# Optimization experiments

Hardware: AMD Instinct MI355X
Metric: run time of the kernel (lower is better)

The kernel has to match this reference:

```python
import jax, jax.numpy as jnp
import numpy as np
from jax import lax

B, CIN, COUT, K, SDIM = 4, 64, 128, 3, 512
D = H = W = 48


def setup_inputs() -> dict:
    key = jax.random.key(0)
    ks = jax.random.split(key, 8)
    inv = lambda n: 1.0 / np.sqrt(n)
    return {
        "x": jax.random.normal(ks[0], (B, CIN, D, H, W), jnp.float32),
        "style": jax.random.normal(ks[1], (B, SDIM), jnp.float32),
        "weight": jax.random.normal(ks[2], (COUT, CIN, K, K, K), jnp.float32),
        "bias": jnp.zeros((COUT,), jnp.float32),
        "w_scale": jax.random.uniform(ks[3], (CIN, SDIM), jnp.float32, -inv(SDIM), inv(SDIM)),
        "b_scale": jnp.zeros((CIN,), jnp.float32),
        "w_shift": jax.random.uniform(ks[4], (CIN, SDIM), jnp.float32, -inv(SDIM), inv(SDIM)),
        "b_shift": jnp.zeros((CIN,), jnp.float32),
        "w_kmod": jax.random.uniform(ks[5], (CIN * K ** 3, SDIM), jnp.float32, -inv(SDIM), inv(SDIM)),
        "b_kmod": jnp.zeros((CIN * K ** 3,), jnp.float32),
    }


def reference(x, style, weight, bias, w_scale, b_scale, w_shift, b_shift, w_kmod, b_kmod):
    # style-based per-channel input modulation: x * (1+scale) + shift
    scale = style @ w_scale.T + b_scale          # [B, CIN]
    shift = style @ w_shift.T + b_shift          # [B, CIN]
    xm = x * (1.0 + scale)[:, :, None, None, None] + shift[:, :, None, None, None]
    # per-sample kernel modulation: weight * (1 + kmod)
    kmod = (style @ w_kmod.T + b_kmod).reshape(B, CIN, K, K, K)
    w = weight[None] * (1.0 + kmod[:, None])     # [B, COUT, CIN, K, K, K]

    def conv_one(xi, wi):
        # xi: [CIN, D, H, W], wi: [COUT, CIN, K, K, K]
        return lax.conv_general_dilated(
            xi[None], wi, window_strides=(1, 1, 1), padding="SAME",
            dimension_numbers=("NCDHW", "OIDHW", "NCDHW"))[0]

    out = jax.vmap(conv_one)(xm, w)              # [B, COUT, D, H, W]
    return out + bias[None, :, None, None, None]
```

## Files before the change

### kernel.cpp

```cpp
#include <hip/hip_runtime.h>
#include <hip/hip_bf16.h>

#define NB   4
#define CIN  64
#define COUT 128
#define SDIM 512
#define DIM  48
#define SP   (DIM*DIM*DIM)
#define TAPS 27
#define KTOT (CIN*TAPS)

#define WS_S1P 0
#define WS_SH  (WS_S1P + NB*CIN)
#define WS_KM  (WS_SH + NB*CIN)
#define XPB_OFF   32768ull
#define XPB_BYTES (4ull*125000ull*64ull*2ull)
#define WSBF_OFF  (XPB_OFF + XPB_BYTES)
#define WSBF_BYTES ((size_t)NB*27*8*128*8*2)

typedef __attribute__((ext_vector_type(4))) float  f32x4;
typedef __attribute__((ext_vector_type(8))) short  short8;
typedef __attribute__((ext_vector_type(8))) unsigned short u16x8;

__global__ void modparams_kernel(const float* __restrict__ style,
                                 const float* __restrict__ w_scale, const float* __restrict__ b_scale,
                                 const float* __restrict__ w_shift, const float* __restrict__ b_shift,
                                 const float* __restrict__ w_kmod,  const float* __restrict__ b_kmod,
                                 float* __restrict__ ws) {
    const int ROWS = 2 * CIN + CIN * TAPS;
    int gwave = (blockIdx.x * blockDim.x + threadIdx.x) >> 6;
    int lane  = threadIdx.x & 63;
    if (gwave >= NB * ROWS) return;
    int b = gwave / ROWS;
    int r = gwave % ROWS;

    const float* srow = style + b * SDIM;
    const float* mrow;
    float bias, add = 0.f;
    float* dst;
    if (r < CIN) {
        mrow = w_scale + r * SDIM; bias = b_scale[r];
        dst = ws + WS_S1P + b * CIN + r; add = 1.f;
    } else if (r < 2 * CIN) {
        int c = r - CIN;
        mrow = w_shift + c * SDIM; bias = b_shift[c];
        dst = ws + WS_SH + b * CIN + c;
    } else {
        int t = r - 2 * CIN;
        mrow = w_kmod + t * SDIM; bias = b_kmod[t];
        dst = ws + WS_KM + b * (CIN * TAPS) + t;
    }

    float acc = 0.f;
    for (int k = lane; k < SDIM; k += 64) acc += srow[k] * mrow[k];
    #pragma unroll
    for (int off = 32; off; off >>= 1) acc += __shfl_down(acc, off);
    if (lane == 0) *dst = acc + bias + add;
}

__global__ void build_wsbf2_kernel(const float* __restrict__ weight, const float* __restrict__ ws,
                                   unsigned short* __restrict__ wsbf) {
    int d = blockIdx.x * blockDim.x + threadIdx.x;
    if (d >= NB * 27 * 8 * 128 * 8) return;
    int j   = d & 7;
    int o   = (d >> 3) & 127;
    int s   = (d >> 10) & 7;
    int rem = d >> 13;
    int tau = rem % 27;
    int b   = rem / 27;
    int c   = s * 8 + j;
    float wm = weight[(o * CIN + c) * TAPS + tau] * (1.f + ws[WS_KM + b * KTOT + c * TAPS + tau]);
    __hip_bfloat16 h = __float2bfloat16(wm);
    wsbf[d] = *(unsigned short*)&h;
}

__global__ __launch_bounds__(256) void pad_kernel(const float* __restrict__ x,
                                                  const float* __restrict__ ws,
                                                  unsigned short* __restrict__ xpb) {
    __shared__ unsigned short lxm[48 * 72];
    int bid = blockIdx.x;
    int py = bid % 50;
    int pz = (bid / 50) % 50;
    int b  = bid / 2500;
    int t = threadIdx.x;
    bool interior = (pz >= 1 && pz <= 48 && py >= 1 && py <= 48);
    if (interior) {
        int z = pz - 1, y = py - 1;
        const float* xr = x + (size_t)b * CIN * SP + (size_t)z * (DIM*DIM) + y * DIM;
        for (int i = t; i < 3072; i += 256) {
            int c = i / 48, w = i % 48;
            float v = xr[(size_t)c * SP + w];
            float m = v * ws[WS_S1P + b * CIN + c] + ws[WS_SH + b * CIN + c];
            __hip_bfloat16 h = __float2bfloat16(m);
            lxm[w * 72 + c] = *(unsigned short*)&h;
        }
    }
    __syncthreads();
    unsigned short* dst = xpb + (size_t)b * 8000000ull + ((size_t)pz * 2500 + py * 50) * 64;
    for (int i8 = t; i8 < 400; i8 += 256) {
        int w  = i8 >> 3;
        int c8 = (i8 & 7) * 8;
        u16x8 v = {};
        if (interior && w >= 1 && w <= 48)
            v = *(const u16x8*)&lxm[(w - 1) * 72 + c8];
        *(u16x8*)(dst + i8 * 8) = v;
    }
}

#define HALOPOS 500
#define PLANE   4008

#define GLD16R(dst, p, OFF)                                                    \
    asm volatile("global_load_dwordx4 %0, %1, off offset:" #OFF                \
                 : "=v"(dst) : "v"(p) : "memory")

#define ISSUEA(buf, tap_) do {                                                 \
    const unsigned short* _p0 = wA + (size_t)(tap_) * 8192;                    \
    const unsigned short* _p1 = _p0 + 4096;                                    \
    GLD16R(buf[0], _p0, 0);   GLD16R(buf[1], _p0, 256);                        \
    GLD16R(buf[2], _p0, 512); GLD16R(buf[3], _p0, 768);                        \
    GLD16R(buf[4], _p1, 0);   GLD16R(buf[5], _p1, 256);                        \
    GLD16R(buf[6], _p1, 512); GLD16R(buf[7], _p1, 768);                        \
} while (0)

#define DLT(t_) (((t_) / 9) * 100 + (((t_) / 3) % 3) * 10 + ((t_) % 3))

#define TAPX(cur, nxt, t_) do {                                                \
    short8 bfr0[4], bfr1[4];                                                   \
    _Pragma("unroll")                                                          \
    for (int nf = 0; nf < 4; ++nf)                                             \
        bfr0[nf] = *(const short8*)&Bh[bOff0 + (DLT(t_) + nf * 20) * 8];       \
    if ((t_) < 26) {                                                           \
        ISSUEA(nxt, (t_) + 1);                                                 \
        asm volatile("s_waitcnt vmcnt(8)" ::: "memory");                       \
    } else {                                                                   \
        asm volatile("s_waitcnt vmcnt(0)" ::: "memory");                       \
    }                                                                          \
    __builtin_amdgcn_sched_barrier(0);                                         \
    __builtin_amdgcn_s_setprio(1);                                             \
    _Pragma("unroll")                                                          \
    for (int mf = 0; mf < 4; ++mf)                                             \
        _Pragma("unroll")                                                      \
        for (int nf = 0; nf < 4; ++nf)                                         \
            acc[mf][nf] = __builtin_amdgcn_mfma_f32_16x16x32_bf16(             \
                cur[mf], bfr0[nf], acc[mf][nf], 0, 0, 0);                      \
    __builtin_amdgcn_s_setprio(0);                                             \
    _Pragma("unroll")                                                          \
    for (int nf = 0; nf < 4; ++nf)                                             \
        bfr1[nf] = *(const short8*)&Bh[bOff1 + (DLT(t_) + nf * 20) * 8];       \
    __builtin_amdgcn_s_setprio(1);                                             \
    _Pragma("unroll")                                                          \
    for (int mf = 0; mf < 4; ++mf)                                             \
        _Pragma("unroll")                                                      \
        for (int nf = 0; nf < 4; ++nf)                                         \
            acc[mf][nf] = __builtin_amdgcn_mfma_f32_16x16x32_bf16(             \
                cur[4 + mf], bfr1[nf], acc[mf][nf], 0, 0, 0);                  \
    __builtin_amdgcn_s_setprio(0);                                             \
} while (0)

__global__ __launch_bounds__(384, 3) void conv_fast8_kernel(
    const unsigned short* __restrict__ xpb,
    const unsigned short* __restrict__ wsbf,
    const float* __restrict__ bias,
    float* __restrict__ out)
{
    __shared__ unsigned short Bh[8 * PLANE];

    const int t    = threadIdx.x;
    const int lane = t & 63;
    const int wid  = t >> 6;
    const int wz   = wid % 3;
    const int mh   = wid / 3;

    int bid0 = blockIdx.x;
    int bid  = (bid0 & 7) * 288 + (bid0 >> 3);
    int tile = bid % 576;
    int b    = bid / 576;
    int tx = tile % 6;
    int ty = (tile / 6) % 6;
    int tz = tile / 36;
    int x0 = tx * 8, y0 = ty * 8, z0 = tz * 3;

    const unsigned short* xb = xpb + (size_t)b * 8000000ull;
    const unsigned short* wb = wsbf + (size_t)b * (27 * 8 * 128 * 8);

    const int col  = lane & 15;
    const int krow = lane >> 4;
    const int cy   = col >> 3;
    const int cx   = col & 7;
    const int pbase = wz * 100 + cy * 10 + cx;

    const int bOff0 = krow * PLANE + pbase * 8;
    const int bOff1 = (4 + krow) * PLANE + pbase * 8;

    const unsigned short* wA = wb + (size_t)(krow * 128 + mh * 64 + col) * 8;

    f32x4 acc[4][4] = {};
    short8 a0[8], a1[8];

    ISSUEA(a0, 0);

    {
        u16x8 stg[11];
        int   li[11];
        #pragma unroll
        for (int it = 0; it < 11; ++it) {
            int i = it * 384 + t;
            li[it] = i;
            if (i < HALOPOS * 8) {
                int pidx = i >> 3;
                int slot = i & 7;
                int hx = pidx % 10;
                int hy = (pidx / 10) % 10;
                int hz = pidx / 100;
                const unsigned short* g = xb
                    + ((size_t)((z0 + hz) * 2500 + (y0 + hy) * 50 + (x0 + hx))) * 64
                    + slot * 8;
                stg[it] = *(const u16x8*)g;
            }
        }
        #pragma unroll
        for (int it = 0; it < 11; ++it) {
            int i = li[it];
            if (i < HALOPOS * 8) {
                int pidx = i >> 3;
                int slot = i & 7;
                *(u16x8*)&Bh[slot * PLANE + pidx * 8] = stg[it];
            }
        }
    }
    __syncthreads();

    #pragma unroll
    for (int tap = 0; tap < 27; ++tap) {
        if ((tap & 1) == 0) TAPX(a0, a1, tap);
        else                TAPX(a1, a0, tap);
    }

    int z  = z0 + wz;
    int xx = x0 + cx;
    #pragma unroll
    for (int mf = 0; mf < 4; ++mf) {
        f32x4 bv = *(const f32x4*)&bias[mh * 64 + mf * 16 + krow * 4];
        #pragma unroll
        for (int nf = 0; nf < 4; ++nf) {
            int y = y0 + nf * 2 + cy;
            size_t p = (size_t)z * (DIM * DIM) + (size_t)y * DIM + xx;
            f32x4 a = acc[mf][nf];
            #pragma unroll
            for (int r = 0; r < 4; ++r) {
                int o = mh * 64 + mf * 16 + krow * 4 + r;
                out[(size_t)(b * COUT + o) * SP + p] = a[r] + bv[r];
            }
        }
    }
}

extern "C" void kernel_launch(void* const* d_in, const int* in_sizes, int n_in,
                              void* d_out, int out_size, void* d_ws, size_t ws_size,
                              hipStream_t stream) {
    const float* x       = (const float*)d_in[0];
    const float* style   = (const float*)d_in[1];
    const float* weight  = (const float*)d_in[2];
    const float* bias    = (const float*)d_in[3];
    const float* w_scale = (const float*)d_in[4];
    const float* b_scale = (const float*)d_in[5];
    const float* w_shift = (const float*)d_in[6];
    const float* b_shift = (const float*)d_in[7];
    const float* w_kmod  = (const float*)d_in[8];
    const float* b_kmod  = (const float*)d_in[9];
    float* out = (float*)d_out;
    float* ws  = (float*)d_ws;

    unsigned short* xpb  = (unsigned short*)((char*)d_ws + XPB_OFF);
    unsigned short* wsbf = (unsigned short*)((char*)d_ws + WSBF_OFF);

    {
        int waves = NB * (2 * CIN + CIN * TAPS);
        int blocks = (waves + 3) / 4;
        modparams_kernel<<<blocks, 256, 0, stream>>>(style, w_scale, b_scale,
                                                     w_shift, b_shift, w_kmod, b_kmod, ws);
    }
    {
        int n = NB * 27 * 8 * 128 * 8;
        build_wsbf2_kernel<<<(n + 255) / 256, 256, 0, stream>>>(weight, ws, wsbf);
    }
    {
        int blocks = NB * 50 * 50;
        pad_kernel<<<blocks, 256, 0, stream>>>(x, ws, xpb);
    }
    {
        int blocks = NB * 576;
        conv_fast8_kernel<<<blocks, 384, 0, stream>>>(xpb, wsbf, bias, out);
    }
}
```

Measured before the change: 236.5 us.

## Enlarge conv tile to 4 z-planes, load halo directly to LDS with XOR swizzle

Each conv block now covers 4 output z-planes with 8 waves (512 threads) instead of 3 planes with 6 waves, so each block amortises more halo and weight traffic. The halo is loaded with global_load_lds straight into shared memory, skipping the register staging pass. The LDS layout becomes position-major with an XOR swizzle on the channel slot, in place of padded channel-slot planes, to avoid bank conflicts. The cost is lower occupancy (2 blocks of 512 threads) and a dependence on the async LDS-load path being correct under a waitcnt-based barrier.

```diff
diff --git a/kernel.cpp b/kernel.cpp
--- a/kernel.cpp
+++ b/kernel.cpp
@@ -21,6 +21,12 @@
 typedef __attribute__((ext_vector_type(4))) float  f32x4;
 typedef __attribute__((ext_vector_type(8))) short  short8;
 typedef __attribute__((ext_vector_type(8))) unsigned short u16x8;
+
+__device__ __forceinline__ void gld16(const void* g, void* l) {
+    __builtin_amdgcn_global_load_lds(
+        (const __attribute__((address_space(1))) void*)g,
+        (__attribute__((address_space(3))) void*)l, 16, 0, 0);
+}
 
 __global__ void modparams_kernel(const float* __restrict__ style,
                                  const float* __restrict__ w_scale, const float* __restrict__ b_scale,
@@ -107,8 +113,8 @@
     }
 }
 
-#define HALOPOS 500
-#define PLANE   4008
+#define HALOPOS 600
+#define BH_CHUNKS (HALOPOS*8)
 
 #define GLD16R(dst, p, OFF)                                                    \
     asm volatile("global_load_dwordx4 %0, %1, off offset:" #OFF                \
@@ -125,11 +131,18 @@
 
 #define DLT(t_) (((t_) / 9) * 100 + (((t_) / 3) % 3) * 10 + ((t_) % 3))
 
+#define BREAD(dst, slotbase, t_) do {                                          \
+    _Pragma("unroll")                                                          \
+    for (int nf = 0; nf < 4; ++nf) {                                           \
+        int pidx = pbase + DLT(t_) + nf * 20;                                  \
+        dst[nf] = *(const short8*)&Bh[pidx * 64 +                              \
+                      (((slotbase) ^ (pidx & 7)) << 3)];                       \
+    }                                                                          \
+} while (0)
+
 #define TAPX(cur, nxt, t_) do {                                                \
     short8 bfr0[4], bfr1[4];                                                   \
-    _Pragma("unroll")                                                          \
-    for (int nf = 0; nf < 4; ++nf)                                             \
-        bfr0[nf] = *(const short8*)&Bh[bOff0 + (DLT(t_) + nf * 20) * 8];       \
+    BREAD(bfr0, krow, t_);                                                     \
     if ((t_) < 26) {                                                           \
         ISSUEA(nxt, (t_) + 1);                                                 \
         asm volatile("s_waitcnt vmcnt(8)" ::: "memory");                       \
@@ -145,9 +158,7 @@
             acc[mf][nf] = __builtin_amdgcn_mfma_f32_16x16x32_bf16(             \
                 cur[mf], bfr0[nf], acc[mf][nf], 0, 0, 0);                      \
     __builtin_amdgcn_s_setprio(0);                                             \
-    _Pragma("unroll")                                                          \
-    for (int nf = 0; nf < 4; ++nf)                                             \
-        bfr1[nf] = *(const short8*)&Bh[bOff1 + (DLT(t_) + nf * 20) * 8];       \
+    BREAD(bfr1, 4 + krow, t_);                                                 \
     __builtin_amdgcn_s_setprio(1);                                             \
     _Pragma("unroll")                                                          \
     for (int mf = 0; mf < 4; ++mf)                                             \
@@ -158,28 +169,28 @@
     __builtin_amdgcn_s_setprio(0);                                             \
 } while (0)
 
-__global__ __launch_bounds__(384, 3) void conv_fast8_kernel(
+__global__ __launch_bounds__(512, 2) void conv_fast10_kernel(
     const unsigned short* __restrict__ xpb,
     const unsigned short* __restrict__ wsbf,
     const float* __restrict__ bias,
     float* __restrict__ out)
 {
-    __shared__ unsigned short Bh[8 * PLANE];
+    __shared__ unsigned short Bh[HALOPOS * 64];
 
     const int t    = threadIdx.x;
     const int lane = t & 63;
     const int wid  = t >> 6;
-    const int wz   = wid % 3;
-    const int mh   = wid / 3;
+    const int wz   = wid & 3;
+    const int mh   = wid >> 2;
 
     int bid0 = blockIdx.x;
-    int bid  = (bid0 & 7) * 288 + (bid0 >> 3);
-    int tile = bid % 576;
-    int b    = bid / 576;
+    int bid  = (bid0 & 7) * 216 + (bid0 >> 3);
+    int tile = bid % 432;
+    int b    = bid / 432;
     int tx = tile % 6;
     int ty = (tile / 6) % 6;
     int tz = tile / 36;
-    int x0 = tx * 8, y0 = ty * 8, z0 = tz * 3;
+    int x0 = tx * 8, y0 = ty * 8, z0 = tz * 4;
 
     const unsigned short* xb = xpb + (size_t)b * 8000000ull;
     const unsigned short* wb = wsbf + (size_t)b * (27 * 8 * 128 * 8);
@@ -190,9 +201,6 @@
     const int cx   = col & 7;
     const int pbase = wz * 100 + cy * 10 + cx;
 
-    const int bOff0 = krow * PLANE + pbase * 8;
-    const int bOff1 = (4 + krow) * PLANE + pbase * 8;
-
     const unsigned short* wA = wb + (size_t)(krow * 128 + mh * 64 + col) * 8;
 
     f32x4 acc[4][4] = {};
@@ -200,33 +208,20 @@
 
     ISSUEA(a0, 0);
 
-    {
-        u16x8 stg[11];
-        int   li[11];
-        #pragma unroll
-        for (int it = 0; it < 11; ++it) {
-            int i = it * 384 + t;
-            li[it] = i;
-            if (i < HALOPOS * 8) {
-                int pidx = i >> 3;
-                int slot = i & 7;
-                int hx = pidx % 10;
-                int hy = (pidx / 10) % 10;
-                int hz = pidx / 100;
-                const unsigned short* g = xb
-                    + ((size_t)((z0 + hz) * 2500 + (y0 + hy) * 50 + (x0 + hx))) * 64
-                    + slot * 8;
-                stg[it] = *(const u16x8*)g;
-            }
-        }
-        #pragma unroll
-        for (int it = 0; it < 11; ++it) {
-            int i = li[it];
-            if (i < HALOPOS * 8) {
-                int pidx = i >> 3;
-                int slot = i & 7;
-                *(u16x8*)&Bh[slot * PLANE + pidx * 8] = stg[it];
-            }
+    #pragma unroll
+    for (int it = 0; it < 10; ++it) {
+        int i = it * 512 + t;
+        if (i < BH_CHUNKS) {
+            int pidx = i >> 3;
+            int slot = i & 7;
+            int hx = pidx % 10;
+            int hy = (pidx / 10) % 10;
+            int hz = pidx / 100;
+            int srcslot = slot ^ (pidx & 7);
+            const unsigned short* g = xb
+                + ((size_t)((z0 + hz) * 2500 + (y0 + hy) * 50 + (x0 + hx))) * 64
+                + srcslot * 8;
+            gld16(g, &Bh[i * 8]);
         }
     }
     __syncthreads();
@@ -290,7 +285,7 @@
         pad_kernel<<<blocks, 256, 0, stream>>>(x, ws, xpb);
     }
     {
-        int blocks = NB * 576;
-        conv_fast8_kernel<<<blocks, 384, 0, stream>>>(xpb, wsbf, bias, out);
-    }
-}
+        int blocks = NB * 432;
+        conv_fast10_kernel<<<blocks, 512, 0, stream>>>(xpb, wsbf, bias, out);
+    }
+}
```

Result: no change. 238.7 us (+0.9%).
